# Kernel tuning notes

Hardware: AMD Instinct MI355X
Metric: run time of the kernel (lower is better)

The kernel has to match this reference:

```python
import jax, jax.numpy as jnp
import numpy as np

B = 16384   # batch
F = 26      # categorical fields
N = 100000  # rows per embedding table
M = 16      # embedding dim per field
NUM = 13    # numerical (dense) features
D = F * M + NUM  # embed_output_dim = 429
L = 6       # CrossNet layers (vector parameterization)
H = 1024    # MLP hidden


def setup_inputs() -> dict:
    key = jax.random.key(0)
    ks = jax.random.split(key, 10)
    Xi = jax.random.randint(ks[0], (B, F, 1), 0, N)
    Xv = jax.random.normal(ks[1], (B, NUM), dtype=jnp.float32)
    # per-field tables, init U(-sqrt(1/n), sqrt(1/n)) as in the torch code; stacked flat
    bound = float(np.sqrt(1.0 / N))
    emb_tables = jax.random.uniform(ks[2], (F * N, M), jnp.float32, -bound, bound)
    cross_w = jax.random.normal(ks[3], (L, D), dtype=jnp.float32) * 0.02
    cross_b = jnp.zeros((L, D), dtype=jnp.float32)
    W1 = jax.random.normal(ks[4], (D, H), dtype=jnp.float32) * (1.0 / np.sqrt(D))
    b1 = jnp.zeros((H,), dtype=jnp.float32)
    W2 = jax.random.normal(ks[5], (H, H), dtype=jnp.float32) * (1.0 / np.sqrt(H))
    b2 = jnp.zeros((H,), dtype=jnp.float32)
    Wout = jax.random.normal(ks[6], (H + D, 1), dtype=jnp.float32) * (1.0 / np.sqrt(H + D))
    bout = jnp.zeros((1,), dtype=jnp.float32)
    return dict(Xi=Xi, Xv=Xv, emb_tables=emb_tables, cross_w=cross_w,
                cross_b=cross_b, W1=W1, b1=b1, W2=W2, b2=b2, Wout=Wout, bout=bout)


def reference(Xi, Xv, emb_tables, cross_w, cross_b, W1, b1, W2, b2, Wout, bout):
    # Fused multi-table EmbeddingBag(mode='sum'): one gather over the stacked tables.
    offs = (jnp.arange(F, dtype=Xi.dtype) * N)[None, :, None]        # [1,F,1]
    flat_idx = (Xi + offs).reshape(-1)                               # [B*F*K]
    g = emb_tables[flat_idx].reshape(B, F, -1, M).sum(axis=2)        # [B,F,M] bag-sum
    x0 = jnp.concatenate([Xv, g.reshape(B, F * M)], axis=1)          # [B,D]
    # CrossNet, vector parameterization: x_{l+1} = x0 * (x_l . w_l) + b_l + x_l
    x = x0
    for l in range(L):
        xw = x @ cross_w[l]                                          # [B]
        x = x0 * xw[:, None] + cross_b[l] + x
    # Deep MLP on x0
    h = jax.nn.relu(x0 @ W1 + b1)
    h = jax.nn.relu(h @ W2 + b2)
    out = jnp.concatenate([h, x], axis=1) @ Wout + bout              # [B,1]
    return out[:, 0]
```

## Files before the change

### kernel.cpp

```cpp
#include <hip/hip_runtime.h>
#include <hip/hip_bf16.h>

#define B_   16384
#define F_   26
#define N_   100000
#define M_   16
#define NUM_ 13
#define D_   429
#define KP1_ 512
#define L_   6
#define H_   1024

typedef unsigned short u16;
typedef __bf16 bf16x8 __attribute__((ext_vector_type(8)));
typedef float  f32x4  __attribute__((ext_vector_type(4)));

__device__ __forceinline__ u16 f2bf_bits(float f) {
  union { float f; unsigned u; } x; x.f = f;
  unsigned r = x.u + 0x7FFFu + ((x.u >> 16) & 1u);
  return (u16)(r >> 16);
}

__global__ __launch_bounds__(256) void fused_front(
    const int* __restrict__ Xi, const float* __restrict__ Xv,
    const float* __restrict__ emb,
    const float* __restrict__ cw, const float* __restrict__ cb,
    const float* __restrict__ Wout, const float* __restrict__ bout,
    const float* __restrict__ W1, const float* __restrict__ W2,
    u16* __restrict__ x0b, u16* __restrict__ w1bt, u16* __restrict__ w2bt,
    float* __restrict__ out) {
  __shared__ __align__(16) u16 sbuf[4][KP1_];
  __shared__ __align__(16) float tile[64][68];
  const int blk = blockIdx.x;
  const int tid = threadIdx.x;
  if (blk < B_ / 4) {
    const int w = tid >> 6, lane = tid & 63;
    const int b = blk * 4 + w;
    const int* xi = Xi + b * F_;

    float x0r[7];
    #pragma unroll
    for (int i = 0; i < 7; ++i) {
      int e = i * 64 + lane;
      float v = 0.f;
      if (e < 416) {
        int f = e >> 4;
        int idx = xi[f];
        v = emb[((size_t)f * N_ + idx) * M_ + (e & 15)];
      } else if (e < D_) {
        v = Xv[b * NUM_ + (e - 416)];
      }
      x0r[i] = v;
      sbuf[w][e] = f2bf_bits(v);
    }
    sbuf[w][448 + lane] = 0;

    float xr[7];
    #pragma unroll
    for (int i = 0; i < 7; ++i) xr[i] = x0r[i];
    for (int l = 0; l < L_; ++l) {
      float wl[7], bl[7];
      #pragma unroll
      for (int i = 0; i < 7; ++i) {
        int e = i * 64 + lane;
        if (e < D_) {
          int d = (e < 416) ? (13 + e) : (e - 416);
          wl[i] = cw[l * D_ + d]; bl[i] = cb[l * D_ + d];
        } else { wl[i] = 0.f; bl[i] = 0.f; }
      }
      float s = 0.f;
      #pragma unroll
      for (int i = 0; i < 7; ++i) s += xr[i] * wl[i];
      #pragma unroll
      for (int off = 32; off; off >>= 1) s += __shfl_xor(s, off);
      #pragma unroll
      for (int i = 0; i < 7; ++i) xr[i] = x0r[i] * s + bl[i] + xr[i];
    }

    __syncthreads();
    ((uint4*)(x0b + (size_t)b * KP1_))[lane] = ((const uint4*)sbuf[w])[lane];

    float s = 0.f;
    #pragma unroll
    for (int i = 0; i < 7; ++i) {
      int e = i * 64 + lane;
      if (e < D_) {
        int d = (e < 416) ? (13 + e) : (e - 416);
        s += xr[i] * Wout[H_ + d];
      }
    }
    #pragma unroll
    for (int off = 32; off; off >>= 1) s += __shfl_xor(s, off);
    if (lane == 0) out[b] = s + bout[0];
  } else {
    int pid = blk - B_ / 4;
    if (pid < 112) {
      const int ti = pid >> 4, tj = pid & 15;
      const int e0 = ti * 64, c0 = tj * 64;
      #pragma unroll
      for (int it = 0; it < 4; ++it) {
        int el = it * 16 + (tid >> 4);
        int e = e0 + el;
        int d = (e < 416) ? (13 + e) : ((e < D_) ? (e - 416) : -1);
        float4 v = make_float4(0.f, 0.f, 0.f, 0.f);
        if (d >= 0) v = *(const float4*)&W1[(size_t)d * H_ + c0 + (tid & 15) * 4];
        *(float4*)&tile[el][(tid & 15) * 4] = v;
      }
      __syncthreads();
      const int nl = tid >> 2, ks = (tid & 3) * 16;
      u16 tmp[16];
      #pragma unroll
      for (int x = 0; x < 16; ++x) tmp[x] = f2bf_bits(tile[ks + x][nl]);
      uint4* dst = (uint4*)&w1bt[(size_t)(c0 + nl) * KP1_ + e0 + ks];
      dst[0] = *(uint4*)&tmp[0];
      dst[1] = *(uint4*)&tmp[8];
    } else {
      pid -= 112;
      const int ti = pid >> 4, tj = pid & 15;
      const int k0 = ti * 64, c0 = tj * 64;
      #pragma unroll
      for (int it = 0; it < 4; ++it) {
        int kl = it * 16 + (tid >> 4);
        *(float4*)&tile[kl][(tid & 15) * 4] =
            *(const float4*)&W2[(size_t)(k0 + kl) * H_ + c0 + (tid & 15) * 4];
      }
      __syncthreads();
      const int nl = tid >> 2, ks = (tid & 3) * 16;
      u16 tmp[16];
      #pragma unroll
      for (int x = 0; x < 16; ++x) tmp[x] = f2bf_bits(tile[ks + x][nl]);
      uint4* dst = (uint4*)&w2bt[(size_t)(c0 + nl) * H_ + k0 + ks];
      dst[0] = *(uint4*)&tmp[0];
      dst[1] = *(uint4*)&tmp[8];
    }
  }
}

#define BARR __builtin_amdgcn_s_barrier()
#define SBR  __builtin_amdgcn_sched_barrier(0)
#define VM6  asm volatile("s_waitcnt vmcnt(6)" ::: "memory")
#define VM0  asm volatile("s_waitcnt vmcnt(0)" ::: "memory")
#define MM(ACC) do { \
  __builtin_amdgcn_s_setprio(1); \
  _Pragma("unroll") \
  for (int mi = 0; mi < 4; ++mi) { \
    _Pragma("unroll") \
    for (int ni = 0; ni < 4; ++ni) \
      ACC[mi][ni] = __builtin_amdgcn_mfma_f32_16x16x32_bf16(af[mi], bfc[ni], ACC[mi][ni], 0, 0, 0); \
  } \
  __builtin_amdgcn_s_setprio(0); \
} while (0)

template<int MODE>
__global__ __launch_bounds__(512, 2) void gemm256(
    const u16* __restrict__ A, const u16* __restrict__ BT,
    const float* __restrict__ bias, u16* __restrict__ C,
    const float* __restrict__ Wout, float* __restrict__ out,
    int N, int K) {
  __shared__ __align__(16) u16 As[2][2][256 * 32];
  __shared__ __align__(16) u16 Bs[2][2][256 * 32];
  const int nbx = N >> 8;
  const int cpx = gridDim.x >> 3;
  const int swz = (blockIdx.x & 7) * cpx + (blockIdx.x >> 3);
  const int bx = swz % nbx;
  const int by = swz / nbx;
  const int tid = threadIdx.x;
  const int l = tid & 63;
  const int w = tid >> 6;
  const int wr = w >> 2, wc = w & 3;
  const int niter = K >> 7;

  const int sr = tid >> 2;
  const int scs = ((tid & 3) ^ ((tid >> 3) & 3)) * 8;
  const u16* gA0 = A  + (size_t)(by * 256 + sr) * K + scs;
  const u16* gB0 = BT + (size_t)(bx * 256 + sr) * K + scs;
  const int dst0 = tid * 8;

  auto stgA = [&](int t, int kk) {
    const u16* s = gA0 + t * 64 + kk * 32;
    __builtin_amdgcn_global_load_lds(
        (const __attribute__((address_space(1))) void*)s,
        (__attribute__((address_space(3))) void*)&As[t & 1][kk][dst0], 16, 0, 0);
    __builtin_amdgcn_global_load_lds(
        (const __attribute__((address_space(1))) void*)(s + (size_t)128 * K),
        (__attribute__((address_space(3))) void*)&As[t & 1][kk][dst0 + 4096], 16, 0, 0);
  };
  auto stgB = [&](int t, int kk) {
    const u16* s = gB0 + t * 64 + kk * 32;
    __builtin_amdgcn_global_load_lds(
        (const __attribute__((address_space(1))) void*)s,
        (__attribute__((address_space(3))) void*)&Bs[t & 1][kk][dst0], 16, 0, 0);
    __builtin_amdgcn_global_load_lds(
        (const __attribute__((address_space(1))) void*)(s + (size_t)128 * K),
        (__attribute__((address_space(3))) void*)&Bs[t & 1][kk][dst0 + 4096], 16, 0, 0);
  };

  const int fr = l & 15, g = l >> 4;
  const int slot = (g ^ ((fr >> 1) & 3)) * 16;
  const int aoff = (wr * 128 + fr) * 64 + slot;
  const int boff = (wc * 64 + fr) * 64 + slot;

  bf16x8 af[4], bfc[4];
  auto rdA = [&](int buf, int kk, int mlo) {
    const char* base = (const char*)&As[buf][kk][0];
    #pragma unroll
    for (int m = 0; m < 4; ++m)
      af[m] = *(const bf16x8*)(base + aoff + (mlo + m) * 1024);
  };
  auto rdB = [&](int buf, int kk) {
    const char* base = (const char*)&Bs[buf][kk][0];
    #pragma unroll
    for (int n = 0; n < 4; ++n)
      bfc[n] = *(const bf16x8*)(base + boff + n * 1024);
  };

  f32x4 accLo[4][4] = {};
  f32x4 accHi[4][4] = {};

  stgA(0, 0); stgB(0, 0); stgA(0, 1); stgB(0, 1);
  stgB(1, 0); stgA(1, 0); stgB(1, 1);
  VM6;
  BARR;

  for (int j = 0; j < niter; ++j) {
    const int t1 = 2 * j + 1;
    const bool stg = (j + 1 < niter);
    rdA(0, 0, 0); rdB(0, 0);
    stgA(t1, 1);
    SBR; BARR; MM(accLo); BARR;
    rdA(0, 0, 4);
    if (stg) stgB(t1 + 1, 0);
    SBR; BARR; MM(accHi); BARR;
    rdA(0, 1, 0); rdB(0, 1);
    if (stg) stgA(t1 + 1, 0);
    SBR; BARR; MM(accLo); BARR;
    rdA(0, 1, 4);
    if (stg) stgB(t1 + 1, 1);
    SBR; BARR; MM(accHi);
    if (stg) { VM6; } else { VM0; }
    BARR;
    rdA(1, 0, 0); rdB(1, 0);
    if (stg) stgA(t1 + 1, 1);
    SBR; BARR; MM(accLo); BARR;
    rdA(1, 0, 4);
    if (stg) stgB(t1 + 2, 0);
    SBR; BARR; MM(accHi); BARR;
    rdA(1, 1, 0); rdB(1, 1);
    if (stg) stgA(t1 + 2, 0);
    SBR; BARR; MM(accLo); BARR;
    rdA(1, 1, 4);
    if (stg) stgB(t1 + 2, 1);
    SBR; BARR; MM(accHi);
    if (stg) { VM6; BARR; }
  }

  const int ccol0 = bx * 256 + wc * 64;
  const int row0 = by * 256 + wr * 128 + g * 4;
  if (MODE == 0) {
    #pragma unroll
    for (int n = 0; n < 4; ++n) {
      int col = ccol0 + n * 16 + fr;
      float bv = bias[col];
      #pragma unroll
      for (int m = 0; m < 4; ++m)
        #pragma unroll
        for (int r = 0; r < 4; ++r) {
          float v0 = fmaxf(accLo[m][n][r] + bv, 0.f);
          C[(size_t)(row0 + m * 16 + r) * N + col] = f2bf_bits(v0);
          float v1 = fmaxf(accHi[m][n][r] + bv, 0.f);
          C[(size_t)(row0 + 64 + m * 16 + r) * N + col] = f2bf_bits(v1);
        }
    }
  } else {
    float bv[4], wv[4];
    #pragma unroll
    for (int n = 0; n < 4; ++n) {
      int col = ccol0 + n * 16 + fr;
      bv[n] = bias[col]; wv[n] = Wout[col];
    }
    #pragma unroll
    for (int m = 0; m < 4; ++m)
      #pragma unroll
      for (int r = 0; r < 4; ++r) {
        float s0 = 0.f, s1 = 0.f;
        #pragma unroll
        for (int n = 0; n < 4; ++n) {
          s0 = fmaf(fmaxf(accLo[m][n][r] + bv[n], 0.f), wv[n], s0);
          s1 = fmaf(fmaxf(accHi[m][n][r] + bv[n], 0.f), wv[n], s1);
        }
        s0 += __shfl_xor(s0, 1); s0 += __shfl_xor(s0, 2);
        s0 += __shfl_xor(s0, 4); s0 += __shfl_xor(s0, 8);
        s1 += __shfl_xor(s1, 1); s1 += __shfl_xor(s1, 2);
        s1 += __shfl_xor(s1, 4); s1 += __shfl_xor(s1, 8);
        if (fr == 0) {
          atomicAdd(out + row0 + m * 16 + r, s0);
          atomicAdd(out + row0 + 64 + m * 16 + r, s1);
        }
      }
  }
}

extern "C" void kernel_launch(void* const* d_in, const int* in_sizes, int n_in,
                              void* d_out, int out_size, void* d_ws, size_t ws_size,
                              hipStream_t stream) {
  const int*   Xi   = (const int*)d_in[0];
  const float* Xv   = (const float*)d_in[1];
  const float* emb  = (const float*)d_in[2];
  const float* cw   = (const float*)d_in[3];
  const float* cb   = (const float*)d_in[4];
  const float* W1   = (const float*)d_in[5];
  const float* b1   = (const float*)d_in[6];
  const float* W2   = (const float*)d_in[7];
  const float* b2   = (const float*)d_in[8];
  const float* Wout = (const float*)d_in[9];
  const float* bout = (const float*)d_in[10];
  float* out = (float*)d_out;

  char* ws = (char*)d_ws;
  size_t off = 0;
  auto alloc = [&](size_t bytes) {
    void* p = ws + off; off += (bytes + 255) & ~(size_t)255; return p;
  };
  u16* x0b  = (u16*)alloc((size_t)B_ * KP1_ * 2);
  u16* w1bt = (u16*)alloc((size_t)H_ * KP1_ * 2);
  u16* w2bt = (u16*)alloc((size_t)H_ * H_ * 2);
  u16* h1   = (u16*)alloc((size_t)B_ * H_ * 2);

  hipLaunchKernelGGL(fused_front, dim3(B_ / 4 + 112 + 256), dim3(256), 0, stream,
                     Xi, Xv, emb, cw, cb, Wout, bout, W1, W2, x0b, w1bt, w2bt, out);
  hipLaunchKernelGGL((gemm256<0>), dim3((B_ / 256) * (H_ / 256)), dim3(512), 0, stream,
                     x0b, w1bt, b1, h1, nullptr, nullptr, H_, KP1_);
  hipLaunchKernelGGL((gemm256<1>), dim3((B_ / 256) * (H_ / 256)), dim3(512), 0, stream,
                     h1, w2bt, b2, nullptr, Wout, out, H_, H_);
}
```

Measured before the change: 94.63 us.

## Trim first GEMM K padding to 448 and restructure GEMM loop per k-tile

The padded K of the first-layer activation buffer drops from 512 to 448, which removes 64 zero columns of MFMA work and global loads from the first GEMM. The GEMM main loop now iterates over single 64-wide k-tiles instead of pairs, so it can handle K values that are odd multiples of 64. The scheduling barriers between LDS reads and MFMA blocks are also removed, leaving instruction interleaving to the compiler. Risks are weaker control over overlap without the sched barriers, and a need for the W1 transpose/padding code (not shown) to match the new stride.

```diff
diff --git a/kernel.cpp b/kernel.cpp
--- a/kernel.cpp
+++ b/kernel.cpp
@@ -7,7 +7,7 @@
 #define M_   16
 #define NUM_ 13
 #define D_   429
-#define KP1_ 512
+#define KP1_ 448
 #define L_   6
 #define H_   1024
 
@@ -53,7 +53,6 @@
       x0r[i] = v;
       sbuf[w][e] = f2bf_bits(v);
     }
-    sbuf[w][448 + lane] = 0;
 
     float xr[7];
     #pragma unroll
@@ -78,7 +77,8 @@
     }
 
     __syncthreads();
-    ((uint4*)(x0b + (size_t)b * KP1_))[lane] = ((const uint4*)sbuf[w])[lane];
+    if (lane < 56)
+      ((uint4*)(x0b + (size_t)b * KP1_))[lane] = ((const uint4*)sbuf[w])[lane];
 
     float s = 0.f;
     #pragma unroll
@@ -137,7 +137,6 @@
 }
 
 #define BARR __builtin_amdgcn_s_barrier()
-#define SBR  __builtin_amdgcn_sched_barrier(0)
 #define VM6  asm volatile("s_waitcnt vmcnt(6)" ::: "memory")
 #define VM0  asm volatile("s_waitcnt vmcnt(0)" ::: "memory")
 #define MM(ACC) do { \
@@ -168,7 +167,7 @@
   const int l = tid & 63;
   const int w = tid >> 6;
   const int wr = w >> 2, wc = w & 3;
-  const int niter = K >> 7;
+  const int nkt = K >> 6;
 
   const int sr = tid >> 2;
   const int scs = ((tid & 3) ^ ((tid >> 3) & 3)) * 8;
@@ -218,40 +217,28 @@
   f32x4 accHi[4][4] = {};
 
   stgA(0, 0); stgB(0, 0); stgA(0, 1); stgB(0, 1);
-  stgB(1, 0); stgA(1, 0); stgB(1, 1);
+  stgA(1, 0); stgB(1, 0); stgB(1, 1);
   VM6;
   BARR;
 
-  for (int j = 0; j < niter; ++j) {
-    const int t1 = 2 * j + 1;
-    const bool stg = (j + 1 < niter);
-    rdA(0, 0, 0); rdB(0, 0);
-    stgA(t1, 1);
-    SBR; BARR; MM(accLo); BARR;
-    rdA(0, 0, 4);
-    if (stg) stgB(t1 + 1, 0);
-    SBR; BARR; MM(accHi); BARR;
-    rdA(0, 1, 0); rdB(0, 1);
-    if (stg) stgA(t1 + 1, 0);
-    SBR; BARR; MM(accLo); BARR;
-    rdA(0, 1, 4);
-    if (stg) stgB(t1 + 1, 1);
-    SBR; BARR; MM(accHi);
-    if (stg) { VM6; } else { VM0; }
-    BARR;
-    rdA(1, 0, 0); rdB(1, 0);
-    if (stg) stgA(t1 + 1, 1);
-    SBR; BARR; MM(accLo); BARR;
-    rdA(1, 0, 4);
-    if (stg) stgB(t1 + 2, 0);
-    SBR; BARR; MM(accHi); BARR;
-    rdA(1, 1, 0); rdB(1, 1);
-    if (stg) stgA(t1 + 2, 0);
-    SBR; BARR; MM(accLo); BARR;
-    rdA(1, 1, 4);
-    if (stg) stgB(t1 + 2, 1);
-    SBR; BARR; MM(accHi);
-    if (stg) { VM6; BARR; }
+  for (int t = 0; t < nkt; ++t) {
+    const int buf = t & 1;
+    const bool s1 = (t + 1 < nkt);
+    const bool s2 = (t + 2 < nkt);
+    rdA(buf, 0, 0); rdB(buf, 0);
+    if (s1) stgA(t + 1, 1);
+    BARR; MM(accLo); BARR;
+    rdA(buf, 0, 4);
+    if (s2) stgB(t + 2, 0);
+    BARR; MM(accHi); BARR;
+    rdA(buf, 1, 0); rdB(buf, 1);
+    if (s2) stgA(t + 2, 0);
+    BARR; MM(accLo); BARR;
+    rdA(buf, 1, 4);
+    if (s2) stgB(t + 2, 1);
+    BARR; MM(accHi);
+    if (s2)      { VM6; BARR; }
+    else if (s1) { VM0; BARR; }
   }
 
   const int ccol0 = bx * 256 + wc * 64;
@@ -282,19 +269,19 @@
     for (int m = 0; m < 4; ++m)
       #pragma unroll
       for (int r = 0; r < 4; ++r) {
-        float s0 = 0.f, s1 = 0.f;
+        float s0 = 0.f, s1v = 0.f;
         #pragma unroll
         for (int n = 0; n < 4; ++n) {
-          s0 = fmaf(fmaxf(accLo[m][n][r] + bv[n], 0.f), wv[n], s0);
-          s1 = fmaf(fmaxf(accHi[m][n][r] + bv[n], 0.f), wv[n], s1);
+          s0  = fmaf(fmaxf(accLo[m][n][r] + bv[n], 0.f), wv[n], s0);
+          s1v = fmaf(fmaxf(accHi[m][n][r] + bv[n], 0.f), wv[n], s1v);
         }
         s0 += __shfl_xor(s0, 1); s0 += __shfl_xor(s0, 2);
         s0 += __shfl_xor(s0, 4); s0 += __shfl_xor(s0, 8);
-        s1 += __shfl_xor(s1, 1); s1 += __shfl_xor(s1, 2);
-        s1 += __shfl_xor(s1, 4); s1 += __shfl_xor(s1, 8);
+        s1v += __shfl_xor(s1v, 1); s1v += __shfl_xor(s1v, 2);
+        s1v += __shfl_xor(s1v, 4); s1v += __shfl_xor(s1v, 8);
         if (fr == 0) {
           atomicAdd(out + row0 + m * 16 + r, s0);
-          atomicAdd(out + row0 + 64 + m * 16 + r, s1);
+          atomicAdd(out + row0 + 64 + m * 16 + r, s1v);
         }
       }
   }
```

New measurement: 95.01 us. Within noise of the previous version (+0.4%).
